# Optimization experiments

Hardware: AMD Instinct MI355X
Metric: run time of the kernel (lower is better)

Reference implementation:

```python
import jax, jax.numpy as jnp
import numpy as np

N, E, F, H, EF, ED, L, NL, NH, OD = 2048, 65536, 128, 512, 16, 64, 5, 4, 8, 64
MAX_DEG = 64


def _ln(x, s, b):
    m = x.mean(-1, keepdims=True)
    v = x.var(-1, keepdims=True)
    return (x - m) * jax.lax.rsqrt(v + 1e-5) * s + b


def setup_inputs() -> dict:
    key = jax.random.key(0)
    ks = jax.random.split(key, 40)
    s = 0.02
    x = jax.random.normal(ks[0], (N, F), jnp.float32)
    edge_index = jax.random.randint(ks[1], (2, E), 0, N, jnp.int32)
    edge_attr = jax.random.normal(ks[2], (E, EF), jnp.float32)
    # variable-length shortest paths, padded with -1
    plen = jax.random.randint(ks[3], (N, N), 0, L + 1, jnp.int32)
    pos = jnp.arange(L, dtype=jnp.int32)
    valid = pos[None, None, :] < plen[:, :, None]
    node_paths = jnp.where(valid, jax.random.randint(ks[4], (N, N, L), 0, N, jnp.int32), -1)
    edge_paths = jnp.where(valid, jax.random.randint(ks[5], (N, N, L), 0, E, jnp.int32), -1)
    p = {
        'x': x, 'edge_index': edge_index, 'edge_attr': edge_attr,
        'node_paths': node_paths, 'edge_paths': edge_paths,
        'W_node': s * jax.random.normal(ks[6], (F, H)), 'b_node': jnp.zeros((H,)),
        'W_edge': s * jax.random.normal(ks[7], (EF, ED)), 'b_edge': jnp.zeros((ED,)),
        'z_in': s * jax.random.normal(ks[8], (MAX_DEG, H)),
        'z_out': s * jax.random.normal(ks[9], (MAX_DEG, H)),
        'b_spatial': s * jax.random.normal(ks[10], (L,)),
        'edge_vector': s * jax.random.normal(ks[11], (L, ED)),
        'ln1_s': jnp.ones((NL, H)), 'ln1_b': jnp.zeros((NL, H)),
        'Wq': s * jax.random.normal(ks[12], (NL, H, H)), 'bq': jnp.zeros((NL, H)),
        'Wk': s * jax.random.normal(ks[13], (NL, H, H)), 'bk': jnp.zeros((NL, H)),
        'Wv': s * jax.random.normal(ks[14], (NL, H, H)), 'bv': jnp.zeros((NL, H)),
        'Wo': s * jax.random.normal(ks[15], (NL, H, H)), 'bo': jnp.zeros((NL, H)),
        'ln2_s': jnp.ones((NL, H)), 'ln2_b': jnp.zeros((NL, H)),
        'W1': s * jax.random.normal(ks[16], (NL, H, H)), 'b1': jnp.zeros((NL, H)),
        'W2': s * jax.random.normal(ks[17], (NL, H, H)), 'b2': jnp.zeros((NL, H)),
        'W_out': s * jax.random.normal(ks[18], (H, OD)), 'b_out': jnp.zeros((OD,)),
    }
    return p


def reference(x, edge_index, edge_attr, node_paths, edge_paths,
              W_node, b_node, W_edge, b_edge, z_in, z_out, b_spatial, edge_vector,
              ln1_s, ln1_b, Wq, bq, Wk, bk, Wv, bv, Wo, bo,
              ln2_s, ln2_b, W1, b1, W2, b2, W_out, b_out):
    n = x.shape[0]
    dk = H // NH
    h = x @ W_node + b_node  # [N,H]
    # centrality encoding: in/out degree -> learned embeddings, clamped
    in_deg = jnp.clip(jnp.zeros((n,), jnp.int32).at[edge_index[1]].add(1), 0, MAX_DEG - 1)
    out_deg = jnp.clip(jnp.zeros((n,), jnp.int32).at[edge_index[0]].add(1), 0, MAX_DEG - 1)
    h = h + z_in[in_deg] + z_out[out_deg]
    # edge encoding: mean over path of <edge_vector[k], edge_emb[path_k]>
    e_emb = edge_attr @ W_edge + b_edge           # [E,ED]
    w = e_emb @ edge_vector.T                     # [E,L] per-position dot products
    valid_e = edge_paths >= 0
    gath = w[jnp.clip(edge_paths, 0), jnp.arange(L)[None, None, :]]  # [N,N,L]
    cnt = valid_e.sum(-1).astype(h.dtype)
    c = jnp.where(cnt > 0, (gath * valid_e).sum(-1) / jnp.maximum(cnt, 1.0), 0.0)  # [N,N]
    # spatial encoding: learned scalar per path length
    plen = (node_paths >= 0).sum(-1)
    b_sp = jnp.where(plen > 0, b_spatial[jnp.clip(plen - 1, 0, L - 1)], 0.0)  # [N,N]
    bias = b_sp + c
    scale = 1.0 / jnp.sqrt(jnp.asarray(dk, h.dtype))
    for l in range(NL):
        y = _ln(h, ln1_s[l], ln1_b[l])
        q = (y @ Wq[l] + bq[l]).reshape(n, NH, dk)
        k = (y @ Wk[l] + bk[l]).reshape(n, NH, dk)
        v = (y @ Wv[l] + bv[l]).reshape(n, NH, dk)
        scores = jnp.einsum('ihd,jhd->hij', q, k) * scale + bias[None]
        attn = jax.nn.softmax(scores, axis=-1)
        o = jnp.einsum('hij,jhd->ihd', attn, v).reshape(n, H)
        h = h + o @ Wo[l] + bo[l]
        y2 = _ln(h, ln2_s[l], ln2_b[l])
        h = h + jax.nn.gelu(y2 @ W1[l] + b1[l]) @ W2[l] + b2[l]
    return h @ W_out + b_out
```

## Files before the change

### kernel.cpp

```cpp
#include <hip/hip_runtime.h>
#include <hip/hip_bf16.h>
#include <math.h>

#define N_NODES 2048
#define NEDGE   65536
#define FDIM    128
#define HDIM    512
#define EFD     16
#define EDD     64
#define LPATH   5
#define NLAYER  4
#define NHEAD   8
#define DK      64
#define ODIM    64
#define MAXDEG  64

typedef __bf16 bf16;
typedef bf16 bf16x8 __attribute__((ext_vector_type(8)));
typedef bf16 bf16x4 __attribute__((ext_vector_type(4)));
typedef float f32x4 __attribute__((ext_vector_type(4)));


__global__ void k_edge_mat(const float* __restrict__ W_edge, const float* __restrict__ b_edge,
                           const float* __restrict__ ev, float* __restrict__ M, float* __restrict__ c5) {
    int t = threadIdx.x;
    if (t < EFD * LPATH) {
        int i = t / LPATH, j = t % LPATH;
        float acc = 0.f;
        for (int k = 0; k < EDD; ++k) acc += W_edge[i * EDD + k] * ev[j * EDD + k];
        M[t] = acc;
    } else if (t >= 80 && t < 80 + LPATH) {
        int j = t - 80;
        float acc = 0.f;
        for (int k = 0; k < EDD; ++k) acc += b_edge[k] * ev[j * EDD + k];
        c5[j] = acc;
    }
}

__global__ __launch_bounds__(256) void k_edge_w(const float* __restrict__ ea, const float* __restrict__ M,
                                                const float* __restrict__ c5, bf16* __restrict__ w) {
    __shared__ float sM[80];
    __shared__ float sc[8];
    int t = threadIdx.x;
    if (t < 80) sM[t] = M[t];
    if (t < LPATH) sc[t] = c5[t];
    __syncthreads();
    int e = blockIdx.x * 256 + t;
    const float4* p = (const float4*)(ea + (size_t)e * EFD);
    float4 a0 = p[0], a1 = p[1], a2 = p[2], a3 = p[3];
    float a[16] = {a0.x, a0.y, a0.z, a0.w, a1.x, a1.y, a1.z, a1.w,
                   a2.x, a2.y, a2.z, a2.w, a3.x, a3.y, a3.z, a3.w};
    float out[LPATH];
#pragma unroll
    for (int j = 0; j < LPATH; ++j) out[j] = sc[j];
#pragma unroll
    for (int i = 0; i < 16; ++i)
#pragma unroll
        for (int j = 0; j < LPATH; ++j) out[j] += a[i] * sM[i * LPATH + j];
#pragma unroll
    for (int j = 0; j < LPATH; ++j) w[(size_t)e * LPATH + j] = (bf16)out[j];
}

__global__ __launch_bounds__(256) void k_deg(const int* __restrict__ ei, int* __restrict__ din, int* __restrict__ dout) {
    int e = blockIdx.x * 256 + threadIdx.x;
    if (e < NEDGE) {
        atomicAdd(&dout[ei[e]], 1);
        atomicAdd(&din[ei[NEDGE + e]], 1);
    }
}

__global__ __launch_bounds__(256) void k_node_proj(const float* __restrict__ x, const float* __restrict__ Wn,
                                                   const float* __restrict__ bn, const float* __restrict__ zin,
                                                   const float* __restrict__ zout, const int* __restrict__ din,
                                                   const int* __restrict__ dout, float* __restrict__ h) {
    __shared__ float xs[FDIM];
    int i = blockIdx.x, t = threadIdx.x;
    if (t < FDIM) xs[t] = x[(size_t)i * FDIM + t];
    __syncthreads();
    int di = min(din[i], MAXDEG - 1), dz = min(dout[i], MAXDEG - 1);
    for (int j = t; j < HDIM; j += 256) {
        float acc = bn[j] + zin[(size_t)di * HDIM + j] + zout[(size_t)dz * HDIM + j];
        for (int k = 0; k < FDIM; ++k) acc += xs[k] * Wn[(size_t)k * HDIM + j];
        h[(size_t)i * HDIM + j] = acc;
    }
}

__global__ __launch_bounds__(256) void k_bias(const int* __restrict__ ep, const bf16* __restrict__ w,
                                              const float* __restrict__ bsp, bf16* __restrict__ bias) {
    __shared__ float sb[5];
    int t = threadIdx.x;
    if (t < 5) sb[t] = bsp[t];
    __syncthreads();
    size_t tid = (size_t)blockIdx.x * 256 + t;
    const int4* p = (const int4*)(ep + tid * 20);
    int4 q0 = p[0], q1 = p[1], q2 = p[2], q3 = p[3], q4 = p[4];
    int e[20] = {q0.x, q0.y, q0.z, q0.w, q1.x, q1.y, q1.z, q1.w,
                 q2.x, q2.y, q2.z, q2.w, q3.x, q3.y, q3.z, q3.w,
                 q4.x, q4.y, q4.z, q4.w};
    bf16x4 out;
#pragma unroll
    for (int pp = 0; pp < 4; ++pp) {
        int cnt = 0;
        float cs = 0.f;
#pragma unroll
        for (int l = 0; l < LPATH; ++l) {
            int ev = e[pp * 5 + l];
            if (ev >= 0) { cnt++; cs += (float)w[(size_t)ev * LPATH + l]; }
        }
        float b = (cnt > 0) ? sb[cnt - 1] + cs / (float)cnt : 0.f;
        out[pp] = (bf16)b;
    }
    *(bf16x4*)(bias + tid * 4) = out;
}

__global__ __launch_bounds__(256) void k_ln(const float* __restrict__ h, const float* __restrict__ sc,
                                            const float* __restrict__ bi, bf16* __restrict__ y) {
    int i = blockIdx.x, t = threadIdx.x;
    float v0 = h[(size_t)i * HDIM + t];
    float v1 = h[(size_t)i * HDIM + 256 + t];
    float s = v0 + v1, q = v0 * v0 + v1 * v1;
#pragma unroll
    for (int m = 1; m < 64; m <<= 1) { s += __shfl_xor(s, m); q += __shfl_xor(q, m); }
    __shared__ float ssum[4], sq[4];
    int wv = t >> 6;
    if ((t & 63) == 0) { ssum[wv] = s; sq[wv] = q; }
    __syncthreads();
    float S = ssum[0] + ssum[1] + ssum[2] + ssum[3];
    float Q = sq[0] + sq[1] + sq[2] + sq[3];
    float mean = S * (1.f / HDIM);
    float var = Q * (1.f / HDIM) - mean * mean;
    float r = rsqrtf(var + 1e-5f);
    y[(size_t)i * HDIM + t] = (bf16)((v0 - mean) * r * sc[t] + bi[t]);
    y[(size_t)i * HDIM + 256 + t] = (bf16)((v1 - mean) * r * sc[256 + t] + bi[256 + t]);
}

__global__ __launch_bounds__(256) void k_wprep(const float* __restrict__ Wq, const float* __restrict__ Wk,
                                               const float* __restrict__ Wv, const float* __restrict__ Wo,
                                               const float* __restrict__ W1, const float* __restrict__ W2,
                                               bf16* __restrict__ Wt) {
    __shared__ float Ls[64][68];
    int m = blockIdx.y;
    int lay = m / 6, type = m % 6;
    const float* src = type == 0 ? Wq : type == 1 ? Wk : type == 2 ? Wv : type == 3 ? Wo : type == 4 ? W1 : W2;
    src += (size_t)lay * (HDIM * HDIM);
    int q = blockIdx.x;
    int tk = q >> 3, tn = q & 7;
    int t = threadIdx.x;
    int rr = t >> 4, cc = t & 15;
#pragma unroll
    for (int u = 0; u < 4; ++u) {
        float4 v = *(const float4*)(src + (size_t)(tk * 64 + rr + 16 * u) * HDIM + tn * 64 + cc * 4);
        *(float4*)&Ls[rr + 16 * u][cc * 4] = v;
    }
    __syncthreads();
    int nl = t >> 2, kc = t & 3;
    bf16 tmp[16];
#pragma unroll
    for (int u = 0; u < 16; ++u) tmp[u] = (bf16)Ls[kc * 16 + u][nl];
    bf16* dst = Wt + (size_t)m * (HDIM * HDIM) + (size_t)(tn * 64 + nl) * HDIM + tk * 64 + kc * 16;
    *(bf16x8*)(dst) = *(bf16x8*)&tmp[0];
    *(bf16x8*)(dst + 8) = *(bf16x8*)&tmp[8];
}

__global__ __launch_bounds__(256) void k_qkv(const bf16* __restrict__ A, const bf16* __restrict__ Wt_l,
                                             const float* __restrict__ bq, const float* __restrict__ bk,
                                             const float* __restrict__ bv, bf16* __restrict__ qf,
                                             bf16* __restrict__ kf, bf16* __restrict__ vf) {
    __shared__ bf16 Bs[16384];
    int t = threadIdx.x, w = t >> 6, l = t & 63, lr = l & 15, lg = l >> 4;
    int j0 = blockIdx.x * 32, i0 = blockIdx.y * 64;
    int type = j0 >> 9, n0 = j0 & 511;
    const bf16* Bp = Wt_l + (size_t)type * (HDIM * HDIM) + (size_t)n0 * HDIM;
#pragma unroll
    for (int rnd = 0; rnd < 8; ++rnd) {
        int tt = rnd * 256 + t;
        int ks = tt >> 7, qq = (tt >> 6) & 1, mm = (tt >> 2) & 15, gg = tt & 3;
        bf16x8 v = *(const bf16x8*)(Bp + (size_t)(qq * 16 + mm) * HDIM + ks * 32 + gg * 8);
        *(bf16x8*)(Bs + tt * 8) = v;
    }
    __syncthreads();
    const bf16* ap = A + (size_t)(i0 + w * 16 + lr) * HDIM + 8 * lg;
    const float* bvec = (type == 0 ? bq : type == 1 ? bk : bv);
    f32x4 acc[2] = {};
#pragma unroll 4
    for (int ks = 0; ks < 16; ++ks) {
        bf16x8 a  = *(const bf16x8*)(ap + ks * 32);
        const bf16* bb = Bs + ks * 1024 + lr * 32 + lg * 8;
        bf16x8 b0 = *(const bf16x8*)(bb);
        bf16x8 b1 = *(const bf16x8*)(bb + 512);
        acc[0] = __builtin_amdgcn_mfma_f32_16x16x32_bf16(a, b0, acc[0], 0, 0, 0);
        acc[1] = __builtin_amdgcn_mfma_f32_16x16x32_bf16(a, b1, acc[1], 0, 0, 0);
    }
    int h = n0 >> 6;
    if (type < 2) {
        bf16* dst = (type == 0 ? qf : kf);
        int hf = (n0 & 32) >> 5;
        float sc = (type == 0 ? 0.125f : 1.0f);
#pragma unroll
        for (int sub = 0; sub < 2; ++sub) {
#pragma unroll
            for (int r = 0; r < 4; ++r) {
                int i = i0 + w * 16 + lg * 4 + r;
                float v = (acc[sub][r] + bvec[n0 + sub * 16 + lr]) * sc;
                int lgp = sub * 2 + (lr >> 3);
                size_t off = (((size_t)(h * 128 + (i >> 4)) * 2 + hf) << 9) + lgp * 128 + (lg * 4 + r) * 8 + (lr & 7);
                dst[off] = (bf16)v;
            }
        }
    } else {
#pragma unroll
        for (int sub = 0; sub < 2; ++sub) {
#pragma unroll
            for (int r = 0; r < 4; ++r) {
                int node = i0 + w * 16 + lg * 4 + r;
                int dd = (n0 & 63) + sub * 16 + lr;
                float v = acc[sub][r] + bvec[n0 + sub * 16 + lr];
                size_t off = (((size_t)(h * 4 + (dd >> 4)) * 64 + (node >> 5)) << 9)
                           + ((node >> 3) & 3) * 128 + (dd & 15) * 8 + (node & 7);
                vf[off] = (bf16)v;
            }
        }
    }
}

#define FL_RES   1
#define FL_GELU  2
#define FL_OUTF  4

__device__ inline float gelu_f(float x) {
    float x3 = x * x * x;
    float u = 0.7978845608028654f * (x + 0.044715f * x3);
    return 0.5f * x * (1.f + tanhf(u));
}

__global__ __launch_bounds__(1024) void k_mm(const bf16* __restrict__ A, const bf16* __restrict__ Bt,
                                             const float* __restrict__ bvec, const float* __restrict__ res,
                                             float* __restrict__ outF, bf16* __restrict__ outB, int flags) {
    __shared__ bf16 Bs[32768];
    __shared__ float Osh[4][16][68];
    int t = threadIdx.x, w = t >> 6, l = t & 63, lr = l & 15, lg = l >> 4;
    int ti = w & 3, s = w >> 2;
    int j0 = blockIdx.x * 64, i0 = blockIdx.y * 64;
    const bf16* Bp = Bt + (size_t)j0 * HDIM;
#pragma unroll
    for (int rnd = 0; rnd < 4; ++rnd) {
        int tt = rnd * 1024 + t;
        int ks = tt >> 8, qq = (tt >> 6) & 3, mm = (tt >> 2) & 15, gg = tt & 3;
        bf16x8 v = *(const bf16x8*)(Bp + (size_t)(qq * 16 + mm) * HDIM + ks * 32 + gg * 8);
        *(bf16x8*)(Bs + tt * 8) = v;
    }
    __syncthreads();
    const bf16* ap = A + (size_t)(i0 + ti * 16 + lr) * HDIM + 8 * lg;
    f32x4 acc[4] = {};
#pragma unroll
    for (int kk = 0; kk < 4; ++kk) {
        int ks = s * 4 + kk;
        bf16x8 a = *(const bf16x8*)(ap + ks * 32);
        const bf16* bb = Bs + ks * 2048 + lr * 32 + lg * 8;
#pragma unroll
        for (int sub = 0; sub < 4; ++sub) {
            bf16x8 b = *(const bf16x8*)(bb + sub * 512);
            acc[sub] = __builtin_amdgcn_mfma_f32_16x16x32_bf16(a, b, acc[sub], 0, 0, 0);
        }
    }
    if (s == 0) {
#pragma unroll
        for (int sub = 0; sub < 4; ++sub)
#pragma unroll
            for (int r = 0; r < 4; ++r) Osh[ti][lg * 4 + r][sub * 16 + lr] = acc[sub][r];
    }
    __syncthreads();
    if (s == 1) {
#pragma unroll
        for (int sub = 0; sub < 4; ++sub)
#pragma unroll
            for (int r = 0; r < 4; ++r) Osh[ti][lg * 4 + r][sub * 16 + lr] += acc[sub][r];
    }
    __syncthreads();
    if (s == 2) {
#pragma unroll
        for (int sub = 0; sub < 4; ++sub)
#pragma unroll
            for (int r = 0; r < 4; ++r) Osh[ti][lg * 4 + r][sub * 16 + lr] += acc[sub][r];
    }
    __syncthreads();
    if (s == 3) {
#pragma unroll
        for (int sub = 0; sub < 4; ++sub) {
#pragma unroll
            for (int r = 0; r < 4; ++r) {
                int i = i0 + ti * 16 + lg * 4 + r;
                int j = j0 + sub * 16 + lr;
                float v = Osh[ti][lg * 4 + r][sub * 16 + lr] + acc[sub][r] + bvec[j];
                if (flags & FL_RES) v += res[(size_t)i * HDIM + j];
                if (flags & FL_GELU) v = gelu_f(v);
                if (flags & FL_OUTF) outF[(size_t)i * HDIM + j] = v;
                else outB[(size_t)i * HDIM + j] = (bf16)v;
            }
        }
    }
}

__global__ __launch_bounds__(1024) void k_attn2(const bf16* __restrict__ qf, const bf16* __restrict__ kf,
                                                const bf16* __restrict__ vf, const bf16* __restrict__ biasb,
                                                bf16* __restrict__ ob) {
    __shared__ char Pb[16 * 1024];
    __shared__ float Osh[4][64][17];
    __shared__ float Msh[4][4][16], Lsh[4][4][16];
    int t = threadIdx.x, w = t >> 6, l = t & 63, lr = l & 15, lg = l >> 4;
    int ti = w & 3, s = w >> 2;
    int bid = blockIdx.x;
    int wid = (bid & 7) * 32 + (bid >> 3);
    int i0 = (wid >> 3) * 64, hh = wid & 7;
    int irow = i0 + ti * 16;

    const bf16* qb = qf + (((size_t)(hh * 128 + (irow >> 4)) * 2) << 9) + l * 8;
    bf16x8 qy0 = *(const bf16x8*)(qb);
    bf16x8 qy1 = *(const bf16x8*)(qb + 512);

    char* pwr = Pb + w * 1024 + lr * 64;
    unsigned kx = (unsigned)(lr & 6) << 3;

    float m_run = -3e38f, l_run = 0.f;
    f32x4 oacc[4] = {};

    for (int it = 0; it < 16; ++it) {
        int jb = s * 512 + it * 32;
        const bf16* kb = kf + (((size_t)(hh * 128 + (jb >> 4)) * 2) << 9) + l * 8;
        bf16x8 kx00 = *(const bf16x8*)(kb);
        bf16x8 kx01 = *(const bf16x8*)(kb + 512);
        bf16x8 kx10 = *(const bf16x8*)(kb + 1024);
        bf16x8 kx11 = *(const bf16x8*)(kb + 1536);
        const bf16* vb = vf + (((size_t)(hh * 4) * 64 + (jb >> 5)) << 9) + l * 8;
        bf16x8 vx0 = *(const bf16x8*)(vb);
        bf16x8 vx1 = *(const bf16x8*)(vb + 32768);
        bf16x8 vx2 = *(const bf16x8*)(vb + 65536);
        bf16x8 vx3 = *(const bf16x8*)(vb + 98304);
        const bf16* bp = biasb + (size_t)(irow + lr) * N_NODES + jb + lg * 4;
        bf16x4 bv0 = *(const bf16x4*)(bp);
        bf16x4 bv1 = *(const bf16x4*)(bp + 16);

        f32x4 s0v = {}, s1v = {};
        s0v = __builtin_amdgcn_mfma_f32_16x16x32_bf16(kx00, qy0, s0v, 0, 0, 0);
        s0v = __builtin_amdgcn_mfma_f32_16x16x32_bf16(kx01, qy1, s0v, 0, 0, 0);
        s1v = __builtin_amdgcn_mfma_f32_16x16x32_bf16(kx10, qy0, s1v, 0, 0, 0);
        s1v = __builtin_amdgcn_mfma_f32_16x16x32_bf16(kx11, qy1, s1v, 0, 0, 0);

        float p0[4], p1[4];
        float mt = -3e38f;
#pragma unroll
        for (int r = 0; r < 4; ++r) {
            p0[r] = s0v[r] + (float)bv0[r];
            p1[r] = s1v[r] + (float)bv1[r];
            mt = fmaxf(mt, fmaxf(p0[r], p1[r]));
        }
        mt = fmaxf(mt, __shfl_xor(mt, 16));
        mt = fmaxf(mt, __shfl_xor(mt, 32));
        float mn = fmaxf(m_run, mt);
        float alpha = __expf(m_run - mn);
        m_run = mn;
        float ps = 0.f;
        bf16x4 pk0, pk1;
#pragma unroll
        for (int r = 0; r < 4; ++r) {
            p0[r] = __expf(p0[r] - mn);
            p1[r] = __expf(p1[r] - mn);
            ps += p0[r] + p1[r];
            pk0[r] = (bf16)p0[r];
            pk1[r] = (bf16)p1[r];
        }
        ps += __shfl_xor(ps, 16);
        ps += __shfl_xor(ps, 32);
        l_run = l_run * alpha + ps;

        *(bf16x4*)(pwr + ((lg * 8) ^ kx)) = pk0;
        *(bf16x4*)(pwr + ((32 + lg * 8) ^ kx)) = pk1;
#pragma unroll
        for (int d = 0; d < 4; ++d) oacc[d] *= alpha;
        asm volatile("s_waitcnt lgkmcnt(0)" ::: "memory");
        __builtin_amdgcn_sched_barrier(0x20);
        bf16x8 py = *(bf16x8*)(Pb + w * 1024 + lr * 64 + ((lg * 16) ^ kx));
        oacc[0] = __builtin_amdgcn_mfma_f32_16x16x32_bf16(vx0, py, oacc[0], 0, 0, 0);
        oacc[1] = __builtin_amdgcn_mfma_f32_16x16x32_bf16(vx1, py, oacc[1], 0, 0, 0);
        oacc[2] = __builtin_amdgcn_mfma_f32_16x16x32_bf16(vx2, py, oacc[2], 0, 0, 0);
        oacc[3] = __builtin_amdgcn_mfma_f32_16x16x32_bf16(vx3, py, oacc[3], 0, 0, 0);
    }

    __syncthreads();
    if (lg == 0) { Msh[ti][s][lr] = m_run; Lsh[ti][s][lr] = l_run; }
    __syncthreads();
    float m0 = Msh[ti][0][lr], m1 = Msh[ti][1][lr], m2 = Msh[ti][2][lr], m3 = Msh[ti][3][lr];
    float mtot = fmaxf(fmaxf(m0, m1), fmaxf(m2, m3));
    float l_tot = Lsh[ti][0][lr] * __expf(m0 - mtot) + Lsh[ti][1][lr] * __expf(m1 - mtot)
                + Lsh[ti][2][lr] * __expf(m2 - mtot) + Lsh[ti][3][lr] * __expf(m3 - mtot);
    float fac = __expf(m_run - mtot);
#pragma unroll
    for (int d = 0; d < 4; ++d) oacc[d] *= fac;
    if (s == 0) {
#pragma unroll
        for (int db = 0; db < 4; ++db)
#pragma unroll
            for (int r = 0; r < 4; ++r) Osh[ti][db * 16 + lg * 4 + r][lr] = oacc[db][r];
    }
    __syncthreads();
    if (s == 1) {
#pragma unroll
        for (int db = 0; db < 4; ++db)
#pragma unroll
            for (int r = 0; r < 4; ++r) Osh[ti][db * 16 + lg * 4 + r][lr] += oacc[db][r];
    }
    __syncthreads();
    if (s == 2) {
#pragma unroll
        for (int db = 0; db < 4; ++db)
#pragma unroll
            for (int r = 0; r < 4; ++r) Osh[ti][db * 16 + lg * 4 + r][lr] += oacc[db][r];
    }
    __syncthreads();
    if (s == 3) {
        float inv = 1.f / l_tot;
#pragma unroll
        for (int db = 0; db < 4; ++db) {
            bf16x4 o4;
#pragma unroll
            for (int r = 0; r < 4; ++r)
                o4[r] = (bf16)((Osh[ti][db * 16 + lg * 4 + r][lr] + oacc[db][r]) * inv);
            *(bf16x4*)(ob + (size_t)(irow + lr) * HDIM + hh * DK + db * 16 + lg * 4) = o4;
        }
    }
}

__global__ __launch_bounds__(256) void k_gemm(const float* __restrict__ A, const float* __restrict__ B,
                                              const float* __restrict__ bvec, float* __restrict__ C,
                                              int M, int Nc, int K) {
    __shared__ float As[16][68];
    __shared__ float Bs[16][68];
    int t = threadIdx.x;
    int tm = t >> 4, tn = t & 15;
    int i0 = blockIdx.y * 64, j0 = blockIdx.x * 64;
    int ar = t >> 2, aq = t & 3;
    int br = t >> 4, bq = t & 15;
    float acc[4][4] = {};
    for (int k0 = 0; k0 < K; k0 += 16) {
        float4 av = *(const float4*)(A + (size_t)(i0 + ar) * K + k0 + aq * 4);
        As[aq * 4 + 0][ar] = av.x;
        As[aq * 4 + 1][ar] = av.y;
        As[aq * 4 + 2][ar] = av.z;
        As[aq * 4 + 3][ar] = av.w;
        *(float4*)&Bs[br][bq * 4] = *(const float4*)(B + (size_t)(k0 + br) * Nc + j0 + bq * 4);
        __syncthreads();
#pragma unroll
        for (int k = 0; k < 16; ++k) {
            float4 a4 = *(const float4*)&As[k][tm * 4];
            float4 b4 = *(const float4*)&Bs[k][tn * 4];
            float avv[4] = {a4.x, a4.y, a4.z, a4.w};
            float bvv[4] = {b4.x, b4.y, b4.z, b4.w};
#pragma unroll
            for (int r = 0; r < 4; ++r)
#pragma unroll
                for (int c = 0; c < 4; ++c) acc[r][c] += avv[r] * bvv[c];
        }
        __syncthreads();
    }
#pragma unroll
    for (int r = 0; r < 4; ++r) {
#pragma unroll
        for (int c = 0; c < 4; ++c) {
            int i = i0 + tm * 4 + r;
            int j = j0 + tn * 4 + c;
            C[(size_t)i * Nc + j] = acc[r][c] + bvec[j];
        }
    }
}

extern "C" void kernel_launch(void* const* d_in, const int* in_sizes, int n_in,
                              void* d_out, int out_size, void* d_ws, size_t ws_size,
                              hipStream_t stream) {
    const float* x      = (const float*)d_in[0];
    const int*   ei     = (const int*)d_in[1];
    const float* eattr  = (const float*)d_in[2];
    const int*   epaths = (const int*)d_in[4];
    const float* Wn     = (const float*)d_in[5];
    const float* bn     = (const float*)d_in[6];
    const float* We     = (const float*)d_in[7];
    const float* be     = (const float*)d_in[8];
    const float* zin    = (const float*)d_in[9];
    const float* zout   = (const float*)d_in[10];
    const float* bsp    = (const float*)d_in[11];
    const float* ev     = (const float*)d_in[12];
    const float* ln1s   = (const float*)d_in[13];
    const float* ln1b   = (const float*)d_in[14];
    const float* Wq     = (const float*)d_in[15];
    const float* bq     = (const float*)d_in[16];
    const float* Wk     = (const float*)d_in[17];
    const float* bk     = (const float*)d_in[18];
    const float* Wv     = (const float*)d_in[19];
    const float* bv     = (const float*)d_in[20];
    const float* Wo     = (const float*)d_in[21];
    const float* bo     = (const float*)d_in[22];
    const float* ln2s   = (const float*)d_in[23];
    const float* ln2b   = (const float*)d_in[24];
    const float* W1     = (const float*)d_in[25];
    const float* b1     = (const float*)d_in[26];
    const float* W2     = (const float*)d_in[27];
    const float* b2     = (const float*)d_in[28];
    const float* Wout   = (const float*)d_in[29];
    const float* bout   = (const float*)d_in[30];

    char* base = (char*)d_ws;
    size_t off = 0;
    auto alloc = [&](size_t bytes) { char* p = base + off; off = (off + bytes + 255) & ~(size_t)255; return p; };
    bf16*  bias   = (bf16*)alloc((size_t)N_NODES * N_NODES * 2);
    float* h      = (float*)alloc((size_t)N_NODES * HDIM * 4);
    bf16*  wbuf   = (bf16*)alloc((size_t)NEDGE * LPATH * 2);
    float* Mb     = (float*)alloc(96 * 4);
    float* c5     = (float*)alloc(16 * 4);
    int*   deg    = (int*)alloc(2 * N_NODES * 4);
    bf16*  y_bf   = (bf16*)alloc((size_t)N_NODES * HDIM * 2);
    bf16*  qfb    = (bf16*)alloc((size_t)NHEAD * 128 * 2 * 512 * 2);
    bf16*  kfb    = (bf16*)alloc((size_t)NHEAD * 128 * 2 * 512 * 2);
    bf16*  vfb    = (bf16*)alloc((size_t)NHEAD * 4 * 64 * 512 * 2);
    bf16*  ob_bf  = (bf16*)alloc((size_t)N_NODES * HDIM * 2);
    bf16*  t1_bf  = (bf16*)alloc((size_t)N_NODES * HDIM * 2);
    bf16*  Wt     = (bf16*)alloc((size_t)NLAYER * 6 * HDIM * HDIM * 2);
    int* din = deg;
    int* dout = deg + N_NODES;

    hipMemsetAsync(deg, 0, 2 * N_NODES * sizeof(int), stream);

    k_edge_mat<<<1, 128, 0, stream>>>(We, be, ev, Mb, c5);
    k_edge_w<<<NEDGE / 256, 256, 0, stream>>>(eattr, Mb, c5, wbuf);
    k_deg<<<NEDGE / 256, 256, 0, stream>>>(ei, din, dout);
    k_node_proj<<<N_NODES, 256, 0, stream>>>(x, Wn, bn, zin, zout, din, dout, h);
    k_bias<<<(N_NODES * (size_t)N_NODES) / 1024, 256, 0, stream>>>(epaths, wbuf, bsp, bias);
    k_wprep<<<dim3(64, 24), 256, 0, stream>>>(Wq, Wk, Wv, Wo, W1, W2, Wt);

    dim3 gqkv(48, 32);
    dim3 gmm(8, 32);

    for (int l = 0; l < NLAYER; ++l) {
        const bf16* Wt_l = Wt + (size_t)l * 6 * HDIM * HDIM;
        size_t bOff = (size_t)l * HDIM;
        k_ln<<<N_NODES, 256, 0, stream>>>(h, ln1s + bOff, ln1b + bOff, y_bf);
        k_qkv<<<gqkv, 256, 0, stream>>>(y_bf, Wt_l, bq + bOff, bk + bOff, bv + bOff, qfb, kfb, vfb);
        k_attn2<<<256, 1024, 0, stream>>>(qfb, kfb, vfb, bias, ob_bf);
        k_mm<<<gmm, 1024, 0, stream>>>(ob_bf, Wt_l + (size_t)3 * HDIM * HDIM, bo + bOff, h, h, nullptr, FL_RES | FL_OUTF);
        k_ln<<<N_NODES, 256, 0, stream>>>(h, ln2s + bOff, ln2b + bOff, y_bf);
        k_mm<<<gmm, 1024, 0, stream>>>(y_bf, Wt_l + (size_t)4 * HDIM * HDIM, b1 + bOff, nullptr, nullptr, t1_bf, FL_GELU);
        k_mm<<<gmm, 1024, 0, stream>>>(t1_bf, Wt_l + (size_t)5 * HDIM * HDIM, b2 + bOff, h, h, nullptr, FL_RES | FL_OUTF);
    }
    k_gemm<<<dim3(1, 32), 256, 0, stream>>>(h, Wout, bout, (float*)d_out, N_NODES, ODIM, HDIM);
}
```

Before: 505.8 us.

## Restructure path-bias gather via LDS, MFMA node projection, lazy softmax rescale

Edge-path bias is now computed in two halves. A pack kernel compresses path indices to u16 per position plus a bitmask. A 1024-thread kernel then stages each position's edge weights (stored transposed, 128KB of bf16) in LDS and gathers from there, replacing scattered global reads. The node projection becomes a bf16 MFMA GEMM with pre-transposed weights and casted x. The attention loop gains s_setprio around its MFMAs and skips the online-softmax rescale unless the running max grows by more than 8. Workspace buffers are aliased into one region to reuse memory, which relies on the pack buffers being dead before the weight prep overwrites them.

```diff
diff --git a/kernel.cpp b/kernel.cpp
--- a/kernel.cpp
+++ b/kernel.cpp
@@ -14,11 +14,14 @@
 #define DK      64
 #define ODIM    64
 #define MAXDEG  64
+#define PHALF   2097152
 
 typedef __bf16 bf16;
 typedef bf16 bf16x8 __attribute__((ext_vector_type(8)));
 typedef bf16 bf16x4 __attribute__((ext_vector_type(4)));
 typedef float f32x4 __attribute__((ext_vector_type(4)));
+typedef unsigned short u16;
+typedef u16 u16x4 __attribute__((ext_vector_type(4)));
 
 
 __global__ void k_edge_mat(const float* __restrict__ W_edge, const float* __restrict__ b_edge,
@@ -38,7 +41,7 @@
 }
 
 __global__ __launch_bounds__(256) void k_edge_w(const float* __restrict__ ea, const float* __restrict__ M,
-                                                const float* __restrict__ c5, bf16* __restrict__ w) {
+                                                const float* __restrict__ c5, bf16* __restrict__ wT) {
     __shared__ float sM[80];
     __shared__ float sc[8];
     int t = threadIdx.x;
@@ -58,7 +61,7 @@
 #pragma unroll
         for (int j = 0; j < LPATH; ++j) out[j] += a[i] * sM[i * LPATH + j];
 #pragma unroll
-    for (int j = 0; j < LPATH; ++j) w[(size_t)e * LPATH + j] = (bf16)out[j];
+    for (int j = 0; j < LPATH; ++j) wT[(size_t)j * NEDGE + e] = (bf16)out[j];
 }
 
 __global__ __launch_bounds__(256) void k_deg(const int* __restrict__ ei, int* __restrict__ din, int* __restrict__ dout) {
@@ -69,48 +72,66 @@
     }
 }
 
-__global__ __launch_bounds__(256) void k_node_proj(const float* __restrict__ x, const float* __restrict__ Wn,
-                                                   const float* __restrict__ bn, const float* __restrict__ zin,
-                                                   const float* __restrict__ zout, const int* __restrict__ din,
-                                                   const int* __restrict__ dout, float* __restrict__ h) {
-    __shared__ float xs[FDIM];
-    int i = blockIdx.x, t = threadIdx.x;
-    if (t < FDIM) xs[t] = x[(size_t)i * FDIM + t];
-    __syncthreads();
-    int di = min(din[i], MAXDEG - 1), dz = min(dout[i], MAXDEG - 1);
-    for (int j = t; j < HDIM; j += 256) {
-        float acc = bn[j] + zin[(size_t)di * HDIM + j] + zout[(size_t)dz * HDIM + j];
-        for (int k = 0; k < FDIM; ++k) acc += xs[k] * Wn[(size_t)k * HDIM + j];
-        h[(size_t)i * HDIM + j] = acc;
-    }
-}
-
-__global__ __launch_bounds__(256) void k_bias(const int* __restrict__ ep, const bf16* __restrict__ w,
-                                              const float* __restrict__ bsp, bf16* __restrict__ bias) {
-    __shared__ float sb[5];
-    int t = threadIdx.x;
-    if (t < 5) sb[t] = bsp[t];
-    __syncthreads();
-    size_t tid = (size_t)blockIdx.x * 256 + t;
-    const int4* p = (const int4*)(ep + tid * 20);
+__global__ __launch_bounds__(256) void k_pack(const int* __restrict__ ep, u16* __restrict__ idxp,
+                                              unsigned char* __restrict__ maskp) {
+    int tid4 = blockIdx.x * 256 + threadIdx.x;
+    const int4* p = (const int4*)(ep + (size_t)tid4 * 20);
     int4 q0 = p[0], q1 = p[1], q2 = p[2], q3 = p[3], q4 = p[4];
     int e[20] = {q0.x, q0.y, q0.z, q0.w, q1.x, q1.y, q1.z, q1.w,
                  q2.x, q2.y, q2.z, q2.w, q3.x, q3.y, q3.z, q3.w,
                  q4.x, q4.y, q4.z, q4.w};
-    bf16x4 out;
+    u16x4 out[LPATH];
+    unsigned m[4] = {0, 0, 0, 0};
 #pragma unroll
     for (int pp = 0; pp < 4; ++pp) {
-        int cnt = 0;
-        float cs = 0.f;
 #pragma unroll
         for (int l = 0; l < LPATH; ++l) {
-            int ev = e[pp * 5 + l];
-            if (ev >= 0) { cnt++; cs += (float)w[(size_t)ev * LPATH + l]; }
-        }
-        float b = (cnt > 0) ? sb[cnt - 1] + cs / (float)cnt : 0.f;
-        out[pp] = (bf16)b;
-    }
-    *(bf16x4*)(bias + tid * 4) = out;
+            int v = e[pp * 5 + l];
+            if (v >= 0) m[pp] |= (1u << l);
+            out[l][pp] = (u16)v;
+        }
+    }
+#pragma unroll
+    for (int l = 0; l < LPATH; ++l)
+        *(u16x4*)(idxp + (size_t)l * PHALF + tid4 * 4) = out[l];
+    unsigned packed = m[0] | (m[1] << 8) | (m[2] << 16) | (m[3] << 24);
+    *(unsigned*)(maskp + (size_t)tid4 * 4) = packed;
+}
+
+__global__ __launch_bounds__(1024) void k_bias2(const u16* __restrict__ idxp, const unsigned char* __restrict__ maskp,
+                                                const bf16* __restrict__ wT, const float* __restrict__ bsp,
+                                                bf16* __restrict__ bias) {
+    __shared__ bf16 wsl[NEDGE];
+    int t = threadIdx.x;
+    int base = blockIdx.x * 8192;
+    unsigned char msk[8];
+    float csum[8] = {};
+#pragma unroll
+    for (int r = 0; r < 8; ++r) msk[r] = maskp[base + r * 1024 + t];
+    for (int l = 0; l < LPATH; ++l) {
+        __syncthreads();
+#pragma unroll
+        for (int u = 0; u < 4; ++u) {
+            int o = u * 16384 + t * 16;
+            *(bf16x8*)&wsl[o]     = *(const bf16x8*)&wT[(size_t)l * NEDGE + o];
+            *(bf16x8*)&wsl[o + 8] = *(const bf16x8*)&wT[(size_t)l * NEDGE + o + 8];
+        }
+        u16 ei[8];
+#pragma unroll
+        for (int r = 0; r < 8; ++r) ei[r] = idxp[(size_t)l * PHALF + base + r * 1024 + t];
+        __syncthreads();
+#pragma unroll
+        for (int r = 0; r < 8; ++r) {
+            float v = (float)wsl[ei[r]];
+            csum[r] += ((msk[r] >> l) & 1) ? v : 0.f;
+        }
+    }
+#pragma unroll
+    for (int r = 0; r < 8; ++r) {
+        int cnt = __popc((int)msk[r]);
+        float b = cnt ? bsp[cnt - 1] + csum[r] / (float)cnt : 0.f;
+        bias[base + r * 1024 + t] = (bf16)b;
+    }
 }
 
 __global__ __launch_bounds__(256) void k_ln(const float* __restrict__ h, const float* __restrict__ sc,
@@ -160,6 +181,71 @@
     bf16* dst = Wt + (size_t)m * (HDIM * HDIM) + (size_t)(tn * 64 + nl) * HDIM + tk * 64 + kc * 16;
     *(bf16x8*)(dst) = *(bf16x8*)&tmp[0];
     *(bf16x8*)(dst + 8) = *(bf16x8*)&tmp[8];
+}
+
+__global__ __launch_bounds__(256) void k_wprepn(const float* __restrict__ Wn, bf16* __restrict__ WnT) {
+    __shared__ float Ls[64][68];
+    int b = blockIdx.x;
+    int tk = b >> 3, tn = b & 7;
+    int t = threadIdx.x, rr = t >> 4, cc = t & 15;
+#pragma unroll
+    for (int u = 0; u < 4; ++u) {
+        float4 v = *(const float4*)(Wn + (size_t)(tk * 64 + rr + 16 * u) * HDIM + tn * 64 + cc * 4);
+        *(float4*)&Ls[rr + 16 * u][cc * 4] = v;
+    }
+    __syncthreads();
+    int nl = t >> 2, kc = t & 3;
+    bf16 tmp[16];
+#pragma unroll
+    for (int u = 0; u < 16; ++u) tmp[u] = (bf16)Ls[kc * 16 + u][nl];
+    bf16* dst = WnT + (size_t)(tn * 64 + nl) * FDIM + tk * 64 + kc * 16;
+    *(bf16x8*)dst = *(bf16x8*)&tmp[0];
+    *(bf16x8*)(dst + 8) = *(bf16x8*)&tmp[8];
+}
+
+__global__ __launch_bounds__(256) void k_xcast(const float* __restrict__ x, bf16* __restrict__ xb) {
+    int i = blockIdx.x * 256 + threadIdx.x;
+    float4 v = *(const float4*)(x + (size_t)i * 4);
+    bf16x4 o;
+    o[0] = (bf16)v.x; o[1] = (bf16)v.y; o[2] = (bf16)v.z; o[3] = (bf16)v.w;
+    *(bf16x4*)(xb + (size_t)i * 4) = o;
+}
+
+__global__ __launch_bounds__(256) void k_nmm(const bf16* __restrict__ A, const bf16* __restrict__ Bt,
+                                             const float* __restrict__ bn, const float* __restrict__ zin,
+                                             const float* __restrict__ zout, const int* __restrict__ din,
+                                             const int* __restrict__ dout, float* __restrict__ h) {
+    __shared__ bf16 Bs[8192];
+    int t = threadIdx.x, w = t >> 6, l = t & 63, lr = l & 15, lg = l >> 4;
+    int j0 = blockIdx.x * 64, i0 = blockIdx.y * 64;
+    const bf16* Bp = Bt + (size_t)j0 * FDIM;
+#pragma unroll
+    for (int rnd = 0; rnd < 4; ++rnd) {
+        int tt = rnd * 256 + t;
+        int ks = tt >> 8, qq = (tt >> 6) & 3, mm = (tt >> 2) & 15, gg = tt & 3;
+        *(bf16x8*)(Bs + tt * 8) = *(const bf16x8*)(Bp + (size_t)(qq * 16 + mm) * FDIM + ks * 32 + gg * 8);
+    }
+    __syncthreads();
+    const bf16* ap = A + (size_t)(i0 + w * 16 + lr) * FDIM + 8 * lg;
+    f32x4 acc[4] = {};
+#pragma unroll
+    for (int ks = 0; ks < 4; ++ks) {
+        bf16x8 a = *(const bf16x8*)(ap + ks * 32);
+        const bf16* bb = Bs + ks * 2048 + lr * 32 + lg * 8;
+#pragma unroll
+        for (int sub = 0; sub < 4; ++sub)
+            acc[sub] = __builtin_amdgcn_mfma_f32_16x16x32_bf16(a, *(const bf16x8*)(bb + sub * 512), acc[sub], 0, 0, 0);
+    }
+#pragma unroll
+    for (int r = 0; r < 4; ++r) {
+        int i = i0 + w * 16 + lg * 4 + r;
+        int di = min(din[i], MAXDEG - 1), dz = min(dout[i], MAXDEG - 1);
+#pragma unroll
+        for (int sub = 0; sub < 4; ++sub) {
+            int j = j0 + sub * 16 + lr;
+            h[(size_t)i * HDIM + j] = acc[sub][r] + bn[j] + zin[(size_t)di * HDIM + j] + zout[(size_t)dz * HDIM + j];
+        }
+    }
 }
 
 __global__ __launch_bounds__(256) void k_qkv(const bf16* __restrict__ A, const bf16* __restrict__ Wt_l,
@@ -341,10 +427,12 @@
         bf16x4 bv1 = *(const bf16x4*)(bp + 16);
 
         f32x4 s0v = {}, s1v = {};
+        __builtin_amdgcn_s_setprio(1);
         s0v = __builtin_amdgcn_mfma_f32_16x16x32_bf16(kx00, qy0, s0v, 0, 0, 0);
         s0v = __builtin_amdgcn_mfma_f32_16x16x32_bf16(kx01, qy1, s0v, 0, 0, 0);
         s1v = __builtin_amdgcn_mfma_f32_16x16x32_bf16(kx10, qy0, s1v, 0, 0, 0);
         s1v = __builtin_amdgcn_mfma_f32_16x16x32_bf16(kx11, qy1, s1v, 0, 0, 0);
+        __builtin_amdgcn_s_setprio(0);
 
         float p0[4], p1[4];
         float mt = -3e38f;
@@ -356,34 +444,39 @@
         }
         mt = fmaxf(mt, __shfl_xor(mt, 16));
         mt = fmaxf(mt, __shfl_xor(mt, 32));
-        float mn = fmaxf(m_run, mt);
-        float alpha = __expf(m_run - mn);
-        m_run = mn;
+        if (!__all(mt <= m_run + 8.f)) {
+            float mn = fmaxf(m_run, mt);
+            float alpha = __expf(m_run - mn);
+            l_run *= alpha;
+#pragma unroll
+            for (int d = 0; d < 4; ++d) oacc[d] *= alpha;
+            m_run = mn;
+        }
         float ps = 0.f;
         bf16x4 pk0, pk1;
 #pragma unroll
         for (int r = 0; r < 4; ++r) {
-            p0[r] = __expf(p0[r] - mn);
-            p1[r] = __expf(p1[r] - mn);
+            p0[r] = __expf(p0[r] - m_run);
+            p1[r] = __expf(p1[r] - m_run);
             ps += p0[r] + p1[r];
             pk0[r] = (bf16)p0[r];
             pk1[r] = (bf16)p1[r];
         }
         ps += __shfl_xor(ps, 16);
         ps += __shfl_xor(ps, 32);
-        l_run = l_run * alpha + ps;
+        l_run += ps;
 
         *(bf16x4*)(pwr + ((lg * 8) ^ kx)) = pk0;
         *(bf16x4*)(pwr + ((32 + lg * 8) ^ kx)) = pk1;
-#pragma unroll
-        for (int d = 0; d < 4; ++d) oacc[d] *= alpha;
         asm volatile("s_waitcnt lgkmcnt(0)" ::: "memory");
         __builtin_amdgcn_sched_barrier(0x20);
         bf16x8 py = *(bf16x8*)(Pb + w * 1024 + lr * 64 + ((lg * 16) ^ kx));
+        __builtin_amdgcn_s_setprio(1);
         oacc[0] = __builtin_amdgcn_mfma_f32_16x16x32_bf16(vx0, py, oacc[0], 0, 0, 0);
         oacc[1] = __builtin_amdgcn_mfma_f32_16x16x32_bf16(vx1, py, oacc[1], 0, 0, 0);
         oacc[2] = __builtin_amdgcn_mfma_f32_16x16x32_bf16(vx2, py, oacc[2], 0, 0, 0);
         oacc[3] = __builtin_amdgcn_mfma_f32_16x16x32_bf16(vx3, py, oacc[3], 0, 0, 0);
+        __builtin_amdgcn_s_setprio(0);
     }
 
     __syncthreads();
@@ -512,35 +605,47 @@
     auto alloc = [&](size_t bytes) { char* p = base + off; off = (off + bytes + 255) & ~(size_t)255; return p; };
     bf16*  bias   = (bf16*)alloc((size_t)N_NODES * N_NODES * 2);
     float* h      = (float*)alloc((size_t)N_NODES * HDIM * 4);
-    bf16*  wbuf   = (bf16*)alloc((size_t)NEDGE * LPATH * 2);
+    bf16*  wT     = (bf16*)alloc((size_t)LPATH * NEDGE * 2);
     float* Mb     = (float*)alloc(96 * 4);
     float* c5     = (float*)alloc(16 * 4);
     int*   deg    = (int*)alloc(2 * N_NODES * 4);
-    bf16*  y_bf   = (bf16*)alloc((size_t)N_NODES * HDIM * 2);
-    bf16*  qfb    = (bf16*)alloc((size_t)NHEAD * 128 * 2 * 512 * 2);
-    bf16*  kfb    = (bf16*)alloc((size_t)NHEAD * 128 * 2 * 512 * 2);
-    bf16*  vfb    = (bf16*)alloc((size_t)NHEAD * 4 * 64 * 512 * 2);
-    bf16*  ob_bf  = (bf16*)alloc((size_t)N_NODES * HDIM * 2);
-    bf16*  t1_bf  = (bf16*)alloc((size_t)N_NODES * HDIM * 2);
-    bf16*  Wt     = (bf16*)alloc((size_t)NLAYER * 6 * HDIM * HDIM * 2);
+    bf16*  xbf    = (bf16*)alloc((size_t)N_NODES * FDIM * 2);
+    bf16*  WnT    = (bf16*)alloc((size_t)HDIM * FDIM * 2);
+    char*  region = alloc(26u * 1024 * 1024);
+    u16*   idxp   = (u16*)region;
+    unsigned char* maskp = (unsigned char*)(region + (size_t)LPATH * PHALF * 2);
+    bf16*  Wt     = (bf16*)region;
+    bf16*  y_bf   = Wt + (size_t)NLAYER * 6 * HDIM * HDIM;
+    bf16*  qfb    = y_bf + (size_t)N_NODES * HDIM;
+    bf16*  kfb    = qfb + (size_t)N_NODES * HDIM / 2 * 2;
+    bf16*  vfb    = kfb + (size_t)NHEAD * 128 * 2 * 512;
+    bf16*  ob_bf  = vfb + (size_t)NHEAD * 4 * 64 * 512;
+    bf16*  t1_bf  = ob_bf + (size_t)N_NODES * HDIM;
     int* din = deg;
     int* dout = deg + N_NODES;
 
     hipMemsetAsync(deg, 0, 2 * N_NODES * sizeof(int), stream);
 
     k_edge_mat<<<1, 128, 0, stream>>>(We, be, ev, Mb, c5);
-    k_edge_w<<<NEDGE / 256, 256, 0, stream>>>(eattr, Mb, c5, wbuf);
+    k_edge_w<<<NEDGE / 256, 256, 0, stream>>>(eattr, Mb, c5, wT);
     k_deg<<<NEDGE / 256, 256, 0, stream>>>(ei, din, dout);
-    k_node_proj<<<N_NODES, 256, 0, stream>>>(x, Wn, bn, zin, zout, din, dout, h);
-    k_bias<<<(N_NODES * (size_t)N_NODES) / 1024, 256, 0, stream>>>(epaths, wbuf, bsp, bias);
+
+    for (int half = 0; half < 2; ++half) {
+        k_pack<<<PHALF / 1024, 256, 0, stream>>>(epaths + (size_t)half * PHALF * 5, idxp, maskp);
+        k_bias2<<<256, 1024, 0, stream>>>(idxp, maskp, wT, bsp, bias + (size_t)half * PHALF);
+    }
+
     k_wprep<<<dim3(64, 24), 256, 0, stream>>>(Wq, Wk, Wv, Wo, W1, W2, Wt);
+    k_wprepn<<<16, 256, 0, stream>>>(Wn, WnT);
+    k_xcast<<<(N_NODES * FDIM) / 1024, 256, 0, stream>>>(x, xbf);
+    k_nmm<<<dim3(8, 32), 256, 0, stream>>>(xbf, WnT, bn, zin, zout, din, dout, h);
 
     dim3 gqkv(48, 32);
     dim3 gmm(8, 32);
 
-    for (int l = 0; l < NLAYER; ++l) {
-        const bf16* Wt_l = Wt + (size_t)l * 6 * HDIM * HDIM;
-        size_t bOff = (size_t)l * HDIM;
+    for (int lay = 0; lay < NLAYER; ++lay) {
+        const bf16* Wt_l = Wt + (size_t)lay * 6 * HDIM * HDIM;
+        size_t bOff = (size_t)lay * HDIM;
         k_ln<<<N_NODES, 256, 0, stream>>>(h, ln1s + bOff, ln1b + bOff, y_bf);
         k_qkv<<<gqkv, 256, 0, stream>>>(y_bf, Wt_l, bq + bOff, bk + bOff, bv + bOff, qfb, kfb, vfb);
         k_attn2<<<256, 1024, 0, stream>>>(qfb, kfb, vfb, bias, ob_bf);
```

Result: no change. 501.7 us (-0.8%).
